# Optimization experiments

Hardware: AMD Instinct MI355X
Metric: run time of the kernel (lower is better)

## Reference

```python
import jax, jax.numpy as jnp
import numpy as np

B, S, HID = 1, 2048, 2048
H, HKV, D = 16, 4, 128
GROUPS = H // HKV
SCALE = D ** -0.5


def rotate_half(x):
    x1, x2 = x[..., : x.shape[-1] // 2], x[..., x.shape[-1] // 2 :]
    return jnp.concatenate((-x2, x1), axis=-1)


def setup_inputs() -> dict:
    key = jax.random.key(0)
    ks = jax.random.split(key, 8)
    hidden_states = jax.random.normal(ks[0], (B, S, HID), dtype=jnp.float32)
    # standard RoPE tables, base 10000
    inv_freq = 1.0 / (10000.0 ** (np.arange(0, D, 2, dtype=np.float32) / D))
    t = np.arange(S, dtype=np.float32)
    freqs = np.outer(t, inv_freq)                      # (S, D/2)
    emb = np.concatenate([freqs, freqs], axis=-1)      # (S, D)
    cos = jnp.asarray(np.cos(emb)[None], dtype=jnp.float32)  # (1, S, D)
    sin = jnp.asarray(np.sin(emb)[None], dtype=jnp.float32)
    std = 0.02
    Wq = jax.random.normal(ks[1], (HID, H * D), dtype=jnp.float32) * std
    Wk = jax.random.normal(ks[2], (HID, HKV * D), dtype=jnp.float32) * std
    Wv = jax.random.normal(ks[3], (HID, HKV * D), dtype=jnp.float32) * std
    Wg = jax.random.normal(ks[4], (HID, HKV), dtype=jnp.float32) * std
    Wo = jax.random.normal(ks[5], (H * D, HID), dtype=jnp.float32) * std
    return {"hidden_states": hidden_states, "cos": cos, "sin": sin,
            "Wq": Wq, "Wk": Wk, "Wv": Wv, "Wg": Wg, "Wo": Wo}


def reference(hidden_states, cos, sin, Wq, Wk, Wv, Wg, Wo):
    b, s, _ = hidden_states.shape
    # projections -> (B, heads, S, D)
    q = (hidden_states @ Wq).reshape(b, s, H, D).transpose(0, 2, 1, 3)
    k = (hidden_states @ Wk).reshape(b, s, HKV, D).transpose(0, 2, 1, 3)
    v = (hidden_states @ Wv).reshape(b, s, HKV, D).transpose(0, 2, 1, 3)
    g = (hidden_states @ Wg).transpose(0, 2, 1)                 # (B, HKV, S)
    g = jax.nn.log_sigmoid(g.astype(jnp.float32))
    # RoPE
    c, sn = cos[:, None, :, :], sin[:, None, :, :]
    q = q * c + rotate_half(q) * sn
    k = k * c + rotate_half(k) * sn
    # GQA repeat kv heads
    k = jnp.repeat(k, GROUPS, axis=1)
    v = jnp.repeat(v, GROUPS, axis=1)
    g = jnp.repeat(g, GROUPS, axis=1)                           # (B, H, S)
    # gated power retention, deg=2, parallel (quadratic) form
    G = jnp.cumsum(g, axis=-1)                                  # (B, H, S)
    # decay_ij = exp(G_i - G_j) for j <= i  (<= 1 since logsigmoid < 0)
    logdecay = G[..., :, None] - G[..., None, :]                # (B, H, S, S)
    causal = jnp.tril(jnp.ones((s, s), dtype=bool))
    decay = jnp.where(causal, jnp.exp(logdecay), 0.0)
    qk = jnp.einsum("bhid,bhjd->bhij", q, k) * SCALE
    scores = (qk * qk) * decay                                  # deg=2 power scores
    den = jnp.maximum(jnp.sum(scores, axis=-1, keepdims=True), 1.0)
    out = jnp.einsum("bhij,bhjd->bhid", scores, v) / den        # (B, H, S, D)
    out = out.transpose(0, 2, 1, 3).reshape(b, s, H * D)
    return out @ Wo
```

## Files before the change

### kernel.cpp

```cpp
#include <hip/hip_runtime.h>
#include <hip/hip_bf16.h>

#define S_LEN 2048
#define HID   2048
#define NH    16
#define NKV   4
#define HD    128
#define KVD   512
#define NQKV  3072
#define SCALE2 0.0078125f

typedef __bf16 bf16;
typedef __attribute__((ext_vector_type(8))) __bf16 bf16x8;
typedef __attribute__((ext_vector_type(4))) float f32x4;

__device__ __forceinline__ void gload_lds16(const bf16* g, bf16* l) {
    __builtin_amdgcn_global_load_lds((const __attribute__((address_space(1))) void*)g,
                                     (__attribute__((address_space(3))) void*)l, 16, 0, 0);
}

__global__ __launch_bounds__(256) void cvt_kernel(const float* __restrict__ in,
                                                  bf16* __restrict__ out, int n)
{
    int i = (blockIdx.x * 256 + threadIdx.x) * 8;
    if (i >= n) return;
    const float4* q = (const float4*)&in[i];
    float4 a = q[0], b = q[1];
    bf16x8 r;
    r[0]=(bf16)a.x; r[1]=(bf16)a.y; r[2]=(bf16)a.z; r[3]=(bf16)a.w;
    r[4]=(bf16)b.x; r[5]=(bf16)b.y; r[6]=(bf16)b.z; r[7]=(bf16)b.w;
    *(bf16x8*)&out[i] = r;
}

__global__ __launch_bounds__(256) void transpose_cvt_kernel(const float* __restrict__ W,
                                                            bf16* __restrict__ Wt,
                                                            int K, int N)
{
    __shared__ float Ts[64][65];
    const int kb = blockIdx.x * 64, nb = blockIdx.y * 64;
    const int t = threadIdx.x;
    const int tr = t >> 6, tc = t & 63;
    #pragma unroll
    for (int p = 0; p < 16; ++p) {
        int k = p * 4 + tr;
        Ts[k][tc] = W[(size_t)(kb + k) * N + nb + tc];
    }
    __syncthreads();
    const int nr = t >> 3, kc = t & 7;
    #pragma unroll
    for (int p = 0; p < 2; ++p) {
        int n = p * 32 + nr;
        bf16x8 o;
        #pragma unroll
        for (int x = 0; x < 8; ++x) o[x] = (bf16)Ts[kc * 8 + x][n];
        *(bf16x8*)&Wt[(size_t)(nb + n) * K + kb + kc * 8] = o;
    }
}

__device__ __forceinline__ void gemm128_core(const bf16* __restrict__ A,
                                             const bf16* __restrict__ Bt,
                                             int K, int mb, int nb,
                                             bf16 (*As)[32], bf16 (*Bs)[32],
                                             f32x4 (*acc)[4],
                                             int w, int l16, int quad, int lane)
{
    const int m0 = (w & 1) * 64, n0 = (w >> 1) * 64;
    const int srow = lane >> 2, scol = (lane & 3) * 8;

    for (int kt = 0; kt < K; kt += 32) {
        __syncthreads();
        gload_lds16(&A [(size_t)(mb + w * 32 +      srow) * K + kt + scol], &As[w * 32     ][0]);
        gload_lds16(&A [(size_t)(mb + w * 32 + 16 + srow) * K + kt + scol], &As[w * 32 + 16][0]);
        gload_lds16(&Bt[(size_t)(nb + w * 32 +      srow) * K + kt + scol], &Bs[w * 32     ][0]);
        gload_lds16(&Bt[(size_t)(nb + w * 32 + 16 + srow) * K + kt + scol], &Bs[w * 32 + 16][0]);
        __syncthreads();

        bf16x8 af[4], bfr[4];
        #pragma unroll
        for (int t = 0; t < 4; ++t) af[t]  = *(const bf16x8*)&As[m0 + t * 16 + l16][quad * 8];
        #pragma unroll
        for (int u = 0; u < 4; ++u) bfr[u] = *(const bf16x8*)&Bs[n0 + u * 16 + l16][quad * 8];
        #pragma unroll
        for (int t = 0; t < 4; ++t)
            #pragma unroll
            for (int u = 0; u < 4; ++u)
                acc[t][u] = __builtin_amdgcn_mfma_f32_16x16x32_bf16(af[t], bfr[u], acc[t][u], 0, 0, 0);
    }
}

__global__ __launch_bounds__(256) void gemm_qkv_kernel(const bf16* __restrict__ A,
                                                       const bf16* __restrict__ Wt,
                                                       bf16* __restrict__ qOut,
                                                       bf16* __restrict__ kOut,
                                                       bf16* __restrict__ vOut,
                                                       int M, int K)
{
    __shared__ __attribute__((aligned(16))) bf16 As[128][32];
    __shared__ __attribute__((aligned(16))) bf16 Bs[128][32];
    const int tid = threadIdx.x, w = tid >> 6, lane = tid & 63;
    const int l16 = lane & 15, quad = lane >> 4;
    const int mb = blockIdx.x * 128, nb = blockIdx.y * 128;
    const int m0 = (w & 1) * 64, n0 = (w >> 1) * 64;

    f32x4 acc[4][4] = {};
    gemm128_core(A, Wt, K, mb, nb, As, Bs, acc, w, l16, quad, lane);

    #pragma unroll
    for (int t = 0; t < 4; ++t)
        #pragma unroll
        for (int u = 0; u < 4; ++u)
            #pragma unroll
            for (int r = 0; r < 4; ++r) {
                int row = mb + m0 + t * 16 + quad * 4 + r;
                int col = nb + n0 + u * 16 + l16;
                bf16 val = (bf16)acc[t][u][r];
                if (nb < 2048)       qOut[(size_t)row * HID + col] = val;
                else if (nb < 2560)  kOut[(size_t)row * KVD + (col - 2048)] = val;
                else                 vOut[(size_t)(col - 2560) * S_LEN + row] = val;
            }
}

__global__ __launch_bounds__(256) void gemm128_kernel(const bf16* __restrict__ A,
                                                      const bf16* __restrict__ Bt,
                                                      float* __restrict__ C,
                                                      int M, int N, int K)
{
    __shared__ __attribute__((aligned(16))) bf16 As[128][32];
    __shared__ __attribute__((aligned(16))) bf16 Bs[128][32];
    const int tid = threadIdx.x, w = tid >> 6, lane = tid & 63;
    const int l16 = lane & 15, quad = lane >> 4;
    const int mb = blockIdx.x * 128, nb = blockIdx.y * 128;
    const int m0 = (w & 1) * 64, n0 = (w >> 1) * 64;

    f32x4 acc[4][4] = {};
    gemm128_core(A, Bt, K, mb, nb, As, Bs, acc, w, l16, quad, lane);

    #pragma unroll
    for (int t = 0; t < 4; ++t)
        #pragma unroll
        for (int u = 0; u < 4; ++u)
            #pragma unroll
            for (int r = 0; r < 4; ++r) {
                int row = mb + m0 + t * 16 + quad * 4 + r;
                int col = nb + n0 + u * 16 + l16;
                C[(size_t)row * N + col] = acc[t][u][r];
            }
}

template<int HEADS>
__global__ __launch_bounds__(256) void rope_kernel(bf16* __restrict__ x,
                                                   const float* __restrict__ cosb,
                                                   const float* __restrict__ sinb)
{
    int idx = blockIdx.x * 256 + threadIdx.x;
    int s   = idx / (HEADS * 64);
    int rem = idx % (HEADS * 64);
    int h   = rem >> 6, d = rem & 63;
    size_t base = (size_t)s * (HEADS * 128) + h * 128 + d;
    float x0 = (float)x[base], x1 = (float)x[base + 64];
    float c0 = cosb[s * 128 + d], c1 = cosb[s * 128 + d + 64];
    float n0 = sinb[s * 128 + d], n1 = sinb[s * 128 + d + 64];
    x[base]      = (bf16)(x0 * c0 - x1 * n0);
    x[base + 64] = (bf16)(x1 * c1 + x0 * n1);
}

__global__ __launch_bounds__(64) void gproj_kernel(const float* __restrict__ hs,
                                                   const float* __restrict__ Wg,
                                                   float* __restrict__ graw)
{
    int s = blockIdx.x, lane = threadIdx.x;
    float a0 = 0.f, a1 = 0.f, a2 = 0.f, a3 = 0.f;
    for (int kk = lane; kk < HID; kk += 64) {
        float h = hs[(size_t)s * HID + kk];
        const float* wr = &Wg[kk * 4];
        a0 += h * wr[0]; a1 += h * wr[1];
        a2 += h * wr[2]; a3 += h * wr[3];
    }
    #pragma unroll
    for (int off = 32; off >= 1; off >>= 1) {
        a0 += __shfl_xor(a0, off); a1 += __shfl_xor(a1, off);
        a2 += __shfl_xor(a2, off); a3 += __shfl_xor(a3, off);
    }
    if (lane == 0) {
        float vv[4] = {a0, a1, a2, a3};
        #pragma unroll
        for (int c = 0; c < 4; ++c) {
            float x = vv[c];
            graw[c * S_LEN + s] = fminf(x, 0.f) - log1pf(expf(-fabsf(x)));
        }
    }
}

__global__ __launch_bounds__(256) void cumsum_kernel(const float* __restrict__ graw,
                                                     float* __restrict__ G)
{
    int c = blockIdx.x, t = threadIdx.x;
    __shared__ float sums[256];
    float loc[8];
    float run = 0.f;
    #pragma unroll
    for (int i = 0; i < 8; ++i) { run += graw[c * S_LEN + t * 8 + i]; loc[i] = run; }
    sums[t] = run;
    __syncthreads();
    for (int off = 1; off < 256; off <<= 1) {
        float add = (t >= off) ? sums[t - off] : 0.f;
        __syncthreads();
        sums[t] += add;
        __syncthreads();
    }
    float offset = sums[t] - run;
    #pragma unroll
    for (int i = 0; i < 8; ++i) G[c * S_LEN + t * 8 + i] = offset + loc[i];
}

__global__ __launch_bounds__(256) void attn_kernel(const bf16* __restrict__ q,
                                                   const bf16* __restrict__ k,
                                                   const bf16* __restrict__ vT,
                                                   const float* __restrict__ G,
                                                   bf16* __restrict__ out)
{
    const int qt = gridDim.x - 1 - blockIdx.x;
    const int h = blockIdx.y, kvh = h >> 2;
    const int qb = qt * 64;
    const int tid = threadIdx.x, w = tid >> 6, lane = tid & 63;
    const int l16 = lane & 15, quad = lane >> 4;

    __shared__ __attribute__((aligned(16))) bf16 Ks4[4][64][32];
    __shared__ __attribute__((aligned(16))) bf16 Vt4[2][128][32];
    __shared__ __attribute__((aligned(16))) bf16 Sb[4][16][72];

    bf16x8 qf[4];
    const int qrow = qb + w * 16 + l16;
    #pragma unroll
    for (int kc = 0; kc < 4; ++kc)
        qf[kc] = *(const bf16x8*)&q[(size_t)qrow * HID + h * HD + kc * 32 + quad * 8];

    const int irow = qb + w * 16 + quad * 4;
    float Gq[4];
    #pragma unroll
    for (int r = 0; r < 4; ++r) Gq[r] = G[kvh * S_LEN + irow + r];

    const int sr4 = lane >> 2, sc4 = (lane & 3) * 8;
    const int vkk = w >> 1, vdg = (w & 1) * 4;

    f32x4 acco[8] = {};
    float den[4] = {0.f, 0.f, 0.f, 0.f};

    for (int kt = 0; kt <= qt; ++kt) {
        const int jb = kt * 64;
        __syncthreads();
        #pragma unroll
        for (int rg = 0; rg < 4; ++rg)
            gload_lds16(&k[(size_t)(jb + rg * 16 + sr4) * KVD + kvh * HD + w * 32 + sc4],
                        &Ks4[w][rg * 16][0]);
        #pragma unroll
        for (int it = 0; it < 4; ++it)
            gload_lds16(&vT[(size_t)(kvh * HD + (vdg + it) * 16 + sr4) * S_LEN + jb + vkk * 32 + sc4],
                        &Vt4[vkk][(vdg + it) * 16][0]);
        __syncthreads();

        f32x4 accs[4] = {};
        #pragma unroll
        for (int t = 0; t < 4; ++t)
            #pragma unroll
            for (int kc = 0; kc < 4; ++kc) {
                bf16x8 bfr = *(const bf16x8*)&Ks4[kc][t * 16 + l16][quad * 8];
                accs[t] = __builtin_amdgcn_mfma_f32_16x16x32_bf16(qf[kc], bfr, accs[t], 0, 0, 0);
            }

        const float Gt = G[kvh * S_LEN + jb];
        float sr[4];
        #pragma unroll
        for (int r = 0; r < 4; ++r) sr[r] = SCALE2 * __expf(Gq[r] - Gt);
        #pragma unroll
        for (int t = 0; t < 4; ++t) {
            int j = jb + t * 16 + l16;
            float colF = __expf(fminf(Gt - G[kvh * S_LEN + j], 85.f));
            #pragma unroll
            for (int r = 0; r < 4; ++r) {
                float d0 = accs[t][r];
                float sc = (j <= irow + r) ? d0 * d0 * sr[r] * colF : 0.f;
                den[r] += sc;
                Sb[w][quad * 4 + r][t * 16 + l16] = (bf16)sc;
            }
        }

        #pragma unroll
        for (int kk = 0; kk < 2; ++kk) {
            bf16x8 af = *(const bf16x8*)&Sb[w][l16][kk * 32 + quad * 8];
            #pragma unroll
            for (int dt = 0; dt < 8; ++dt) {
                bf16x8 bfr = *(const bf16x8*)&Vt4[kk][dt * 16 + l16][quad * 8];
                acco[dt] = __builtin_amdgcn_mfma_f32_16x16x32_bf16(af, bfr, acco[dt], 0, 0, 0);
            }
        }
    }

    #pragma unroll
    for (int r = 0; r < 4; ++r) {
        #pragma unroll
        for (int off = 1; off < 16; off <<= 1) den[r] += __shfl_xor(den[r], off);
        den[r] = 1.f / fmaxf(den[r], 1.f);
    }
    #pragma unroll
    for (int dt = 0; dt < 8; ++dt)
        #pragma unroll
        for (int r = 0; r < 4; ++r)
            out[(size_t)(irow + r) * HID + h * HD + dt * 16 + l16] = (bf16)(acco[dt][r] * den[r]);
}

extern "C" void kernel_launch(void* const* d_in, const int* in_sizes, int n_in,
                              void* d_out, int out_size, void* d_ws, size_t ws_size,
                              hipStream_t stream)
{
    const float* hs   = (const float*)d_in[0];
    const float* cosb = (const float*)d_in[1];
    const float* sinb = (const float*)d_in[2];
    const float* Wq   = (const float*)d_in[3];
    const float* Wk   = (const float*)d_in[4];
    const float* Wv   = (const float*)d_in[5];
    const float* Wg   = (const float*)d_in[6];
    const float* Wo   = (const float*)d_in[7];
    float* out = (float*)d_out;

    char* p = (char*)d_ws;
    bf16*  qbuf  = (bf16*)p;  p += (size_t)S_LEN * HID * 2;
    bf16*  kbuf  = (bf16*)p;  p += (size_t)S_LEN * KVD * 2;
    bf16*  vT    = (bf16*)p;  p += (size_t)S_LEN * KVD * 2;
    bf16*  abuf  = (bf16*)p;  p += (size_t)S_LEN * HID * 2;
    bf16*  hsb   = (bf16*)p;  p += (size_t)S_LEN * HID * 2;
    bf16*  WcatT = (bf16*)p;  p += (size_t)NQKV * HID * 2;
    bf16*  WoT   = (bf16*)p;  p += (size_t)HID * HID * 2;
    float* graw  = (float*)p; p += (size_t)NKV * S_LEN * 4;
    float* G     = (float*)p; p += (size_t)NKV * S_LEN * 4;

    cvt_kernel<<<(S_LEN * HID) / (256 * 8), 256, 0, stream>>>(hs, hsb, S_LEN * HID);
    transpose_cvt_kernel<<<dim3(32, 32), 256, 0, stream>>>(Wq, WcatT,                          HID, HID);
    transpose_cvt_kernel<<<dim3(32,  8), 256, 0, stream>>>(Wk, WcatT + (size_t)2048 * HID,     HID, KVD);
    transpose_cvt_kernel<<<dim3(32,  8), 256, 0, stream>>>(Wv, WcatT + (size_t)2560 * HID,     HID, KVD);
    transpose_cvt_kernel<<<dim3(32, 32), 256, 0, stream>>>(Wo, WoT, HID, HID);

    gemm_qkv_kernel<<<dim3(16, 24), 256, 0, stream>>>(hsb, WcatT, qbuf, kbuf, vT, S_LEN, HID);

    gproj_kernel<<<S_LEN, 64, 0, stream>>>(hs, Wg, graw);
    cumsum_kernel<<<NKV, 256, 0, stream>>>(graw, G);
    rope_kernel<NH ><<<(S_LEN * NH  * 64) / 256, 256, 0, stream>>>(qbuf, cosb, sinb);
    rope_kernel<NKV><<<(S_LEN * NKV * 64) / 256, 256, 0, stream>>>(kbuf, cosb, sinb);

    attn_kernel<<<dim3(32, NH), 256, 0, stream>>>(qbuf, kbuf, vT, G, abuf);

    gemm128_kernel<<<dim3(16, 16), 256, 0, stream>>>(abuf, WoT, out, S_LEN, HID, HID);
}
```

Before: 312.3 us.

## Split causal attention along the key axis and split-K the output projection

Attention query tiles are now split into chunks of up to 8 key tiles, giving 80 blocks per head instead of 32 and evening out causal load imbalance. Multi-chunk tiles write fp32 partial outputs and denominators to workspace, and a new reduce kernel sums them and normalizes. The Wo GEMM is split in two along K with atomic adds into a pre-zeroed output, doubling the block count to fill more CUs. The cost is extra partial-buffer traffic, an additional zero kernel and reduce kernel, atomic contention, and non-deterministic fp32 summation order.

```diff
diff --git a/kernel.cpp b/kernel.cpp
--- a/kernel.cpp
+++ b/kernel.cpp
@@ -9,6 +9,7 @@
 #define KVD   512
 #define NQKV  3072
 #define SCALE2 0.0078125f
+#define NCH   80
 
 typedef __bf16 bf16;
 typedef __attribute__((ext_vector_type(8))) __bf16 bf16x8;
@@ -32,6 +33,12 @@
     *(bf16x8*)&out[i] = r;
 }
 
+__global__ __launch_bounds__(256) void zero_kernel(float* __restrict__ p, int n)
+{
+    int i = (blockIdx.x * 256 + threadIdx.x) * 4;
+    if (i < n) *(float4*)&p[i] = make_float4(0.f, 0.f, 0.f, 0.f);
+}
+
 __global__ __launch_bounds__(256) void transpose_cvt_kernel(const float* __restrict__ W,
                                                             bf16* __restrict__ Wt,
                                                             int K, int N)
@@ -59,7 +66,7 @@
 
 __device__ __forceinline__ void gemm128_core(const bf16* __restrict__ A,
                                              const bf16* __restrict__ Bt,
-                                             int K, int mb, int nb,
+                                             int K, int k0, int k1, int mb, int nb,
                                              bf16 (*As)[32], bf16 (*Bs)[32],
                                              f32x4 (*acc)[4],
                                              int w, int l16, int quad, int lane)
@@ -67,7 +74,7 @@
     const int m0 = (w & 1) * 64, n0 = (w >> 1) * 64;
     const int srow = lane >> 2, scol = (lane & 3) * 8;
 
-    for (int kt = 0; kt < K; kt += 32) {
+    for (int kt = k0; kt < k1; kt += 32) {
         __syncthreads();
         gload_lds16(&A [(size_t)(mb + w * 32 +      srow) * K + kt + scol], &As[w * 32     ][0]);
         gload_lds16(&A [(size_t)(mb + w * 32 + 16 + srow) * K + kt + scol], &As[w * 32 + 16][0]);
@@ -103,7 +110,7 @@
     const int m0 = (w & 1) * 64, n0 = (w >> 1) * 64;
 
     f32x4 acc[4][4] = {};
-    gemm128_core(A, Wt, K, mb, nb, As, Bs, acc, w, l16, quad, lane);
+    gemm128_core(A, Wt, K, 0, K, mb, nb, As, Bs, acc, w, l16, quad, lane);
 
     #pragma unroll
     for (int t = 0; t < 4; ++t)
@@ -120,7 +127,7 @@
             }
 }
 
-__global__ __launch_bounds__(256) void gemm128_kernel(const bf16* __restrict__ A,
+__global__ __launch_bounds__(256) void gemm_wo_kernel(const bf16* __restrict__ A,
                                                       const bf16* __restrict__ Bt,
                                                       float* __restrict__ C,
                                                       int M, int N, int K)
@@ -131,9 +138,10 @@
     const int l16 = lane & 15, quad = lane >> 4;
     const int mb = blockIdx.x * 128, nb = blockIdx.y * 128;
     const int m0 = (w & 1) * 64, n0 = (w >> 1) * 64;
+    const int kh = K >> 1, k0 = blockIdx.z * kh;
 
     f32x4 acc[4][4] = {};
-    gemm128_core(A, Bt, K, mb, nb, As, Bs, acc, w, l16, quad, lane);
+    gemm128_core(A, Bt, K, k0, k0 + kh, mb, nb, As, Bs, acc, w, l16, quad, lane);
 
     #pragma unroll
     for (int t = 0; t < 4; ++t)
@@ -143,7 +151,7 @@
             for (int r = 0; r < 4; ++r) {
                 int row = mb + m0 + t * 16 + quad * 4 + r;
                 int col = nb + n0 + u * 16 + l16;
-                C[(size_t)row * N + col] = acc[t][u][r];
+                unsafeAtomicAdd(&C[(size_t)row * N + col], acc[t][u][r]);
             }
 }
 
@@ -217,9 +225,20 @@
                                                    const bf16* __restrict__ k,
                                                    const bf16* __restrict__ vT,
                                                    const float* __restrict__ G,
-                                                   bf16* __restrict__ out)
-{
-    const int qt = gridDim.x - 1 - blockIdx.x;
+                                                   bf16* __restrict__ out,
+                                                   float* __restrict__ pO,
+                                                   float* __restrict__ pden)
+{
+    int rem = blockIdx.x, qt = 0, cch = 0;
+    #pragma unroll
+    for (int g = 0; g < 4; ++g) {
+        int sz = 8 * (g + 1);
+        if (rem < sz) { qt = g * 8 + rem / (g + 1); cch = rem % (g + 1); break; }
+        rem -= sz;
+    }
+    const int gg = qt >> 3, nc = gg + 1;
+    const int jt0 = cch * 8, jt1 = min(qt + 1, jt0 + 8);
+
     const int h = blockIdx.y, kvh = h >> 2;
     const int qb = qt * 64;
     const int tid = threadIdx.x, w = tid >> 6, lane = tid & 63;
@@ -227,7 +246,7 @@
 
     __shared__ __attribute__((aligned(16))) bf16 Ks4[4][64][32];
     __shared__ __attribute__((aligned(16))) bf16 Vt4[2][128][32];
-    __shared__ __attribute__((aligned(16))) bf16 Sb[4][16][72];
+    __shared__ __attribute__((aligned(16))) bf16 Sb[4][16][68];
 
     bf16x8 qf[4];
     const int qrow = qb + w * 16 + l16;
@@ -246,7 +265,7 @@
     f32x4 acco[8] = {};
     float den[4] = {0.f, 0.f, 0.f, 0.f};
 
-    for (int kt = 0; kt <= qt; ++kt) {
+    for (int kt = jt0; kt < jt1; ++kt) {
         const int jb = kt * 64;
         __syncthreads();
         #pragma unroll
@@ -300,13 +319,67 @@
     for (int r = 0; r < 4; ++r) {
         #pragma unroll
         for (int off = 1; off < 16; off <<= 1) den[r] += __shfl_xor(den[r], off);
-        den[r] = 1.f / fmaxf(den[r], 1.f);
-    }
-    #pragma unroll
-    for (int dt = 0; dt < 8; ++dt)
-        #pragma unroll
-        for (int r = 0; r < 4; ++r)
-            out[(size_t)(irow + r) * HID + h * HD + dt * 16 + l16] = (bf16)(acco[dt][r] * den[r]);
+    }
+
+    if (nc == 1) {
+        float dinv[4];
+        #pragma unroll
+        for (int r = 0; r < 4; ++r) dinv[r] = 1.f / fmaxf(den[r], 1.f);
+        #pragma unroll
+        for (int dt = 0; dt < 8; ++dt)
+            #pragma unroll
+            for (int r = 0; r < 4; ++r)
+                out[(size_t)(irow + r) * HID + h * HD + dt * 16 + l16] =
+                    (bf16)(acco[dt][r] * dinv[r]);
+    } else {
+        const int slot = h * NCH + 4 * gg * (gg + 1) + (qt & 7) * (gg + 1) + cch;
+        float* po = &pO[(size_t)slot * 8192];
+        const int lr = w * 16 + quad * 4;
+        #pragma unroll
+        for (int dt = 0; dt < 8; ++dt)
+            #pragma unroll
+            for (int r = 0; r < 4; ++r)
+                po[(lr + r) * 128 + dt * 16 + l16] = acco[dt][r];
+        if (l16 == 0) {
+            #pragma unroll
+            for (int r = 0; r < 4; ++r) pden[slot * 64 + lr + r] = den[r];
+        }
+    }
+}
+
+__global__ __launch_bounds__(256) void attn_reduce_kernel(const float* __restrict__ pO,
+                                                          const float* __restrict__ pden,
+                                                          bf16* __restrict__ out)
+{
+    const int p = blockIdx.x;
+    const int h = p / 24, qt = 8 + p % 24;
+    const int gg = qt >> 3, nc = gg + 1;
+    const int base = h * NCH + 4 * gg * (gg + 1) + (qt & 7) * (gg + 1);
+    const int qb = qt * 64;
+    const int tid = threadIdx.x;
+
+    __shared__ float sden[64];
+    if (tid < 64) {
+        float s = 0.f;
+        for (int c = 0; c < nc; ++c) s += pden[(base + c) * 64 + tid];
+        sden[tid] = 1.f / fmaxf(s, 1.f);
+    }
+    __syncthreads();
+
+    #pragma unroll
+    for (int i = 0; i < 8; ++i) {
+        int e = i * 1024 + tid * 4;
+        float4 s = make_float4(0.f, 0.f, 0.f, 0.f);
+        for (int c = 0; c < nc; ++c) {
+            float4 v = *(const float4*)&pO[(size_t)(base + c) * 8192 + e];
+            s.x += v.x; s.y += v.y; s.z += v.z; s.w += v.w;
+        }
+        int lr = e >> 7, col = e & 127;
+        float di = sden[lr];
+        bf16* o = &out[(size_t)(qb + lr) * HID + h * HD + col];
+        o[0] = (bf16)(s.x * di); o[1] = (bf16)(s.y * di);
+        o[2] = (bf16)(s.z * di); o[3] = (bf16)(s.w * di);
+    }
 }
 
 extern "C" void kernel_launch(void* const* d_in, const int* in_sizes, int n_in,
@@ -333,12 +406,15 @@
     bf16*  WoT   = (bf16*)p;  p += (size_t)HID * HID * 2;
     float* graw  = (float*)p; p += (size_t)NKV * S_LEN * 4;
     float* G     = (float*)p; p += (size_t)NKV * S_LEN * 4;
+    float* pO    = (float*)p; p += (size_t)NH * NCH * 8192 * 4;
+    float* pden  = (float*)p; p += (size_t)NH * NCH * 64 * 4;
 
     cvt_kernel<<<(S_LEN * HID) / (256 * 8), 256, 0, stream>>>(hs, hsb, S_LEN * HID);
-    transpose_cvt_kernel<<<dim3(32, 32), 256, 0, stream>>>(Wq, WcatT,                          HID, HID);
-    transpose_cvt_kernel<<<dim3(32,  8), 256, 0, stream>>>(Wk, WcatT + (size_t)2048 * HID,     HID, KVD);
-    transpose_cvt_kernel<<<dim3(32,  8), 256, 0, stream>>>(Wv, WcatT + (size_t)2560 * HID,     HID, KVD);
+    transpose_cvt_kernel<<<dim3(32, 32), 256, 0, stream>>>(Wq, WcatT,                      HID, HID);
+    transpose_cvt_kernel<<<dim3(32,  8), 256, 0, stream>>>(Wk, WcatT + (size_t)2048 * HID, HID, KVD);
+    transpose_cvt_kernel<<<dim3(32,  8), 256, 0, stream>>>(Wv, WcatT + (size_t)2560 * HID, HID, KVD);
     transpose_cvt_kernel<<<dim3(32, 32), 256, 0, stream>>>(Wo, WoT, HID, HID);
+    zero_kernel<<<(S_LEN * HID) / (256 * 4), 256, 0, stream>>>(out, S_LEN * HID);
 
     gemm_qkv_kernel<<<dim3(16, 24), 256, 0, stream>>>(hsb, WcatT, qbuf, kbuf, vT, S_LEN, HID);
 
@@ -347,7 +423,8 @@
     rope_kernel<NH ><<<(S_LEN * NH  * 64) / 256, 256, 0, stream>>>(qbuf, cosb, sinb);
     rope_kernel<NKV><<<(S_LEN * NKV * 64) / 256, 256, 0, stream>>>(kbuf, cosb, sinb);
 
-    attn_kernel<<<dim3(32, NH), 256, 0, stream>>>(qbuf, kbuf, vT, G, abuf);
-
-    gemm128_kernel<<<dim3(16, 16), 256, 0, stream>>>(abuf, WoT, out, S_LEN, HID, HID);
-}
+    attn_kernel<<<dim3(NCH, NH), 256, 0, stream>>>(qbuf, kbuf, vT, G, abuf, pO, pden);
+    attn_reduce_kernel<<<NH * 24, 256, 0, stream>>>(pO, pden, abuf);
+
+    gemm_wo_kernel<<<dim3(16, 16, 2), 256, 0, stream>>>(abuf, WoT, out, S_LEN, HID, HID);
+}
```

Measured after the change: 310.2 us. No clear change (-0.7%).
